# Kernel tuning notes

Hardware: AMD Instinct MI355X
Metric: run time of the kernel (lower is better)

## Reference

```python
import jax, jax.numpy as jnp
import numpy as np

B, N, DIM_IN, DIM_K, DIM_V, NH = 2, 2048, 1024, 1024, 1024, 16

def setup_inputs() -> dict:
    key = jax.random.key(0)
    ks = jax.random.split(key, 7)
    s_in = 1.0 / np.sqrt(DIM_IN)
    return {
        "x": jax.random.normal(ks[0], (B, N, DIM_IN), dtype=jnp.float32),
        "Wq": jax.random.uniform(ks[1], (DIM_IN, DIM_K), jnp.float32, -s_in, s_in),
        "bq": jax.random.uniform(ks[2], (DIM_K,), jnp.float32, -s_in, s_in),
        "Wk": jax.random.uniform(ks[3], (DIM_IN, DIM_K), jnp.float32, -s_in, s_in),
        "bk": jax.random.uniform(ks[4], (DIM_K,), jnp.float32, -s_in, s_in),
        "Wv": jax.random.uniform(ks[5], (DIM_IN, DIM_V), jnp.float32, -s_in, s_in),
        "bv": jax.random.uniform(ks[6], (DIM_V,), jnp.float32, -s_in, s_in),
    }

def reference(x, Wq, bq, Wk, bk, Wv, bv):
    b, n, _ = x.shape
    dk = DIM_K // NH
    dv = DIM_V // NH
    scale = 1.0 / np.sqrt(dk)
    # project and split heads: [b, nh, n, dk]
    q = (x @ Wq + bq).reshape(b, n, NH, dk).transpose(0, 2, 1, 3)
    k = (x @ Wk + bk).reshape(b, n, NH, dk).transpose(0, 2, 1, 3)
    v = (x @ Wv + bv).reshape(b, n, NH, dv).transpose(0, 2, 1, 3)
    dist = jnp.einsum('bhqd,bhkd->bhqk', q, k) * scale  # [b,nh,n,n]
    dist = jax.nn.softmax(dist, axis=-1)
    att = jnp.einsum('bhqk,bhkd->bhqd', dist, v)
    return att.transpose(0, 2, 1, 3).reshape(b, n, DIM_V)
```

## Files before the change

### kernel.cpp

```cpp
#include <hip/hip_runtime.h>

#define DI __device__ __forceinline__

typedef unsigned short u16;
typedef short short8 __attribute__((ext_vector_type(8)));
typedef float f32x4 __attribute__((ext_vector_type(4)));
typedef float f32x16 __attribute__((ext_vector_type(16)));
typedef u16 u16x4 __attribute__((ext_vector_type(4)));
typedef unsigned u32x4 __attribute__((ext_vector_type(4)));
typedef int i32x2 __attribute__((ext_vector_type(2)));

DI u16 f2bf(float f){
    unsigned u = __builtin_bit_cast(unsigned, f);
    u += 0x7FFFu + ((u >> 16) & 1u);
    return (u16)(u >> 16);
}

#if defined(__has_builtin)
#if __has_builtin(__builtin_amdgcn_global_load_lds)
#define HAS_GLL 1
#endif
#if __has_builtin(__builtin_amdgcn_exp2f)
#define HAS_EXP2 1
#endif
#if __has_builtin(__builtin_amdgcn_permlane32_swap)
#define HAS_PL32 1
#endif
#endif

DI void async16(u16* lds, const u16* g){
#ifdef HAS_GLL
    __builtin_amdgcn_global_load_lds(
        (const __attribute__((address_space(1))) unsigned int*)g,
        (__attribute__((address_space(3))) unsigned int*)lds, 16, 0, 0);
#else
    *(short8*)lds = *(const short8*)g;
#endif
}

DI float ex2(float x){
#ifdef HAS_EXP2
    return __builtin_amdgcn_exp2f(x);
#else
    return exp2f(x);
#endif
}

DI unsigned cvtpk(float lo, float hi){
    unsigned r;
    asm("v_cvt_pk_bf16_f32 %0, %1, %2" : "=v"(r) : "v"(lo), "v"(hi));
    return r;
}

DI i32x2 plswap(int a, int b){
#ifdef HAS_PL32
    return __builtin_amdgcn_permlane32_swap(a, b, false, false);
#else
    i32x2 r;
    int ax = __shfl_xor(a, 32), bx = __shfl_xor(b, 32);
    int hi = (threadIdx.x & 63) >> 5;
    r[0] = hi ? bx : a;
    r[1] = hi ? b : ax;
    return r;
#endif
}

#define SEQ   2048
#define DIN   1024
#define MTOT  4096
#define QSCALE 0.18033688011112042f
#define THR2   11.5f

__global__ void k_cvt_x(const float* __restrict__ x, u16* __restrict__ xb){
    int i = (blockIdx.x * 256 + threadIdx.x) * 4;
    f32x4 v = *(const f32x4*)(x + i);
    u16x4 o;
    for (int j = 0; j < 4; j++) o[j] = f2bf(v[j]);
    *(u16x4*)(xb + i) = o;
}

__global__ void k_tw3(const float* __restrict__ Wq, const float* __restrict__ Wk,
                      const float* __restrict__ Wv, u16* __restrict__ Wt3){
    const float* W = (blockIdx.z == 0) ? Wq : (blockIdx.z == 1) ? Wk : Wv;
    u16* Wt = Wt3 + (size_t)blockIdx.z * DIN * DIN;
    __shared__ float t[32][33];
    int tx = threadIdx.x, ty = threadIdx.y;
    int n0 = blockIdx.x * 32, k0 = blockIdx.y * 32;
    for (int i = 0; i < 4; i++)
        t[ty + i*8][tx] = W[(size_t)(k0 + ty + i*8) * DIN + n0 + tx];
    __syncthreads();
    for (int i = 0; i < 4; i++)
        Wt[(size_t)(n0 + ty + i*8) * DIN + k0 + tx] = f2bf(t[tx][ty + i*8]);
}

__global__ __launch_bounds__(256, 3) void k_projf(const u16* __restrict__ A,
                                                  const u16* __restrict__ Wt3,
                                                  const float* __restrict__ bq,
                                                  const float* __restrict__ bk,
                                                  const float* __restrict__ bv,
                                                  u16* __restrict__ qb,
                                                  u16* __restrict__ kb,
                                                  u16* __restrict__ vtb){
    __shared__ __align__(16) u16 As[3][4096];
    __shared__ __align__(16) u16 Bs[3][4096];
    int tid = threadIdx.x;
    int l = tid & 63, w = tid >> 6;
    int lq = l & 15, lg = l >> 4;
    int wm = w >> 1, wn = w & 1;
    int by  = blockIdx.y;
    int mat = by >> 3;
    int m0 = blockIdx.x * 128, n0 = (by & 7) * 128;
    const u16* Bt = Wt3 + (size_t)mat * DIN * DIN;
    const float* bias = (mat == 0) ? bq : (mat == 1) ? bk : bv;

    int r0 = tid >> 2, c0 = (tid & 3) * 8;
    const u16* ap0 = A  + (size_t)(m0 + r0)      * DIN + c0;
    const u16* ap1 = A  + (size_t)(m0 + 64 + r0) * DIN + c0;
    const u16* bp0 = Bt + (size_t)(n0 + r0)      * DIN + c0;
    const u16* bp1 = Bt + (size_t)(n0 + 64 + r0) * DIN + c0;
    int d0 = tid * 8, d1 = 2048 + tid * 8;

#define PSTAGE(bi) {                                              \
    async16(&As[bi][d0], ap0); async16(&As[bi][d1], ap1);         \
    async16(&Bs[bi][d0], bp0); async16(&Bs[bi][d1], bp1);         \
    ap0 += 32; ap1 += 32; bp0 += 32; bp1 += 32; }

    f32x4 acc[4][4] = {};
    PSTAGE(0)

    for (int t = 0; t < 32; t++){
        int cur = t % 3;
        if (t + 1 < 32){
            PSTAGE((t + 1) % 3)
            asm volatile("s_waitcnt vmcnt(4)" ::: "memory");
        } else {
            asm volatile("s_waitcnt vmcnt(0)" ::: "memory");
        }
        __builtin_amdgcn_s_barrier();

        short8 af[4], bf[4];
        #pragma unroll
        for (int f = 0; f < 4; f++){
            af[f] = *(const short8*)&As[cur][(wm*64 + f*16 + lq) * 32 + lg * 8];
            bf[f] = *(const short8*)&Bs[cur][(wn*64 + f*16 + lq) * 32 + lg * 8];
        }
        #pragma unroll
        for (int fm = 0; fm < 4; fm++)
            #pragma unroll
            for (int fn = 0; fn < 4; fn++)
                acc[fm][fn] = __builtin_amdgcn_mfma_f32_16x16x32_bf16(af[fm], bf[fn], acc[fm][fn], 0, 0, 0);
        __builtin_amdgcn_s_barrier();
    }
#undef PSTAGE

    for (int fn = 0; fn < 4; fn++){
        int cc = n0 + wn*64 + fn*16 + lq;
        float bvv = bias[cc];
        int h = cc >> 6, d = cc & 63;
        for (int fm = 0; fm < 4; fm++){
            int mbase = m0 + wm*64 + fm*16 + lg*4;
            int b = mbase >> 11, n = mbase & 2047;
            if (mat == 2){
                u16x4 pv;
                for (int r = 0; r < 4; r++) pv[r] = f2bf(acc[fm][fn][r] + bvv);
                *(u16x4*)&vtb[((size_t)(b*16 + h) * 64 + d) * SEQ + n] = pv;
            } else {
                u16* dst = (mat == 0) ? qb : kb;
                float sc = (mat == 0) ? QSCALE : 1.0f;
                for (int r = 0; r < 4; r++){
                    float v = (acc[fm][fn][r] + bvv) * sc;
                    dst[((size_t)(b*16 + h) * SEQ + (n + r)) * 64 + d] = f2bf(v);
                }
            }
        }
    }
}

#define MFMA32(a, b, c) __builtin_amdgcn_mfma_f32_32x32x16_bf16(a, b, c, 0, 0, 0)

#define MAKE_PA(dst, S, base) {                                   \
    unsigned a0 = cvtpk(S[base+0], S[base+1]);                    \
    unsigned a1 = cvtpk(S[base+2], S[base+3]);                    \
    unsigned b0 = cvtpk(S[base+4], S[base+5]);                    \
    unsigned b1 = cvtpk(S[base+6], S[base+7]);                    \
    i32x2 r0 = plswap((int)a0, (int)b0);                          \
    i32x2 r1 = plswap((int)a1, (int)b1);                          \
    u32x4 wv = {(unsigned)r0[0], (unsigned)r1[0],                 \
                (unsigned)r0[1], (unsigned)r1[1]};                \
    dst = __builtin_bit_cast(short8, wv); }

template<int SPLIT>
__global__ __launch_bounds__(256, 3) void k_attn(const u16* __restrict__ Q,
                                                 const u16* __restrict__ K,
                                                 const u16* __restrict__ Vt,
                                                 float* __restrict__ out,
                                                 float* __restrict__ po,
                                                 float* __restrict__ mls){
    __shared__ __align__(16) u16 Ks[3][64 * 64];
    __shared__ __align__(16) u16 Vs[3][64 * 64];

    int tid = threadIdx.x, l = tid & 63, w = tid >> 6;
    int lq = l & 31, hi = l >> 5;
    int bh = blockIdx.y;
    int b = bh >> 4, h = bh & 15;
    int q0 = blockIdx.x * 128 + w * 32;
    int sp = blockIdx.z;
    int kvb = sp * (SEQ / SPLIT);
    const int NT = (SEQ / SPLIT) / 64;

    const u16* Qb = Q  + (size_t)bh * SEQ * 64;
    const u16* Kb = K  + (size_t)bh * SEQ * 64;
    const u16* Vb = Vt + (size_t)bh * 64 * SEQ;

    int row0 = tid >> 3;
    int c0   = (tid & 7) ^ (row0 & 7);
    const u16* kp0 = Kb + (size_t)(kvb + row0)      * 64 + c0 * 8;
    const u16* kp1 = Kb + (size_t)(kvb + row0 + 32) * 64 + c0 * 8;
    const u16* vp0 = Vb + (size_t)row0        * SEQ + kvb + c0 * 8;
    const u16* vp1 = Vb + (size_t)(row0 + 32) * SEQ + kvb + c0 * 8;
    int d0 = tid * 8, d1 = 2048 + tid * 8;

#define STAGE(bi) {                                               \
    async16(&Ks[bi][d0], kp0); async16(&Ks[bi][d1], kp1);         \
    async16(&Vs[bi][d0], vp0); async16(&Vs[bi][d1], vp1);         \
    kp0 += 64*64; kp1 += 64*64; vp0 += 64; vp1 += 64; }

    short8 qf[4];
    #pragma unroll
    for (int ks = 0; ks < 4; ks++)
        qf[ks] = *(const short8*)(Qb + (size_t)(q0 + lq) * 64 + ks*16 + hi*8);

    STAGE(0)

    float m = -INFINITY, ls = 0.f;
    f32x16 o0 = {}, o1 = {};
    int rx = (lq & 7) << 4;

    for (int t = 0; t < NT; t++){
        int cur = t % 3;
        if (t + 1 < NT){
            STAGE((t + 1) % 3)
            asm volatile("s_waitcnt vmcnt(4)" ::: "memory");
        } else {
            asm volatile("s_waitcnt vmcnt(0)" ::: "memory");
        }
        __builtin_amdgcn_s_barrier();

        const char* kB = (const char*)&Ks[cur][0];
        const char* vB = (const char*)&Vs[cur][0];

        f32x16 st0 = {}, st1 = {};
        #pragma unroll
        for (int ks = 0; ks < 4; ks++){
            int cb = ((ks*2 + hi) << 4) ^ rx;
            short8 ka = *(const short8*)(kB + lq*128        + cb);
            short8 kb = *(const short8*)(kB + (32+lq)*128   + cb);
            st0 = MFMA32(ka, qf[ks], st0);
            st1 = MFMA32(kb, qf[ks], st1);
        }

        float p0 = fmaxf(st0[0], st1[0]), p1 = fmaxf(st0[1], st1[1]);
        float p2 = fmaxf(st0[2], st1[2]), p3 = fmaxf(st0[3], st1[3]);
        #pragma unroll
        for (int r = 4; r < 16; r += 4){
            p0 = fmaxf(p0, fmaxf(st0[r+0], st1[r+0]));
            p1 = fmaxf(p1, fmaxf(st0[r+1], st1[r+1]));
            p2 = fmaxf(p2, fmaxf(st0[r+2], st1[r+2]));
            p3 = fmaxf(p3, fmaxf(st0[r+3], st1[r+3]));
        }
        float pm = fmaxf(fmaxf(p0, p1), fmaxf(p2, p3));
        pm = fmaxf(pm, __shfl_xor(pm, 32));

        if (__any(pm > m + THR2)){
            float mn  = fmaxf(m, pm);
            float fac = ex2(m - mn);
            m = mn;
            ls *= fac;
            #pragma unroll
            for (int r = 0; r < 16; r++){
                int row = (r & 3) + 8*(r >> 2) + 4*hi;
                float f = __shfl(fac, row);
                o0[r] *= f; o1[r] *= f;
            }
        }

        float psum = 0.f;
        #pragma unroll
        for (int r = 0; r < 16; r++){
            st0[r] = ex2(st0[r] - m); psum += st0[r];
            st1[r] = ex2(st1[r] - m); psum += st1[r];
        }
        psum += __shfl_xor(psum, 32);
        ls += psum;

        short8 pa0, pa1, pa2, pa3;
        MAKE_PA(pa0, st0, 0)
        MAKE_PA(pa1, st0, 8)
        MAKE_PA(pa2, st1, 0)
        MAKE_PA(pa3, st1, 8)

        #pragma unroll
        for (int kct = 0; kct < 4; kct++){
            short8 pf = (kct == 0) ? pa0 : (kct == 1) ? pa1 : (kct == 2) ? pa2 : pa3;
            int cb = ((kct*2 + hi) << 4) ^ rx;
            short8 v0 = *(const short8*)(vB + lq*128      + cb);
            short8 v1 = *(const short8*)(vB + (32+lq)*128 + cb);
            o0 = MFMA32(pf, v0, o0);
            o1 = MFMA32(pf, v1, o1);
        }
        __builtin_amdgcn_s_barrier();
    }

    if (SPLIT == 1){
        #pragma unroll
        for (int r = 0; r < 16; r++){
            int row = (r & 3) + 8*(r >> 2) + 4*hi;
            float inv = 1.0f / __shfl(ls, row);
            float* op = out + ((size_t)b * SEQ + (q0 + row)) * 1024 + h*64 + lq;
            op[0]  = o0[r] * inv;
            op[32] = o1[r] * inv;
        }
    } else {
        float* pb = po + (size_t)sp * MTOT * 1024;
        #pragma unroll
        for (int r = 0; r < 16; r++){
            int row = (r & 3) + 8*(r >> 2) + 4*hi;
            float* op = pb + ((size_t)b * SEQ + (q0 + row)) * 1024 + h*64 + lq;
            op[0]  = o0[r];
            op[32] = o1[r];
        }
        if (hi == 0){
            float* mp = mls + (((size_t)sp*32 + bh) * SEQ + (q0 + lq)) * 2;
            mp[0] = m; mp[1] = ls;
        }
    }
#undef STAGE
}

template<int S>
__global__ __launch_bounds__(256) void k_comb(const float* __restrict__ po,
                                              const float* __restrict__ mls,
                                              float* __restrict__ out){
    size_t i = ((size_t)blockIdx.x * 256 + threadIdx.x) * 4;
    size_t row = i >> 10;
    int col = (int)(i & 1023);
    int b = (int)(row >> 11), n = (int)(row & 2047);
    int bh = b*16 + (col >> 6);

    float mv[S], lv[S], wv[S];
    float M = -INFINITY;
    #pragma unroll
    for (int s = 0; s < S; s++){
        const float* p = mls + (((size_t)s*32 + bh) * SEQ + n) * 2;
        mv[s] = p[0]; lv[s] = p[1];
        M = fmaxf(M, mv[s]);
    }
    float L = 0.f;
    #pragma unroll
    for (int s = 0; s < S; s++){ wv[s] = ex2(mv[s] - M); L += wv[s] * lv[s]; }
    float inv = 1.0f / L;
    f32x4 acc = {};
    #pragma unroll
    for (int s = 0; s < S; s++){
        f32x4 v = *(const f32x4*)(po + (size_t)s * MTOT * 1024 + i);
        acc += v * wv[s];
    }
    acc *= inv;
    *(f32x4*)(out + i) = acc;
}

extern "C" void kernel_launch(void* const* d_in, const int* in_sizes, int n_in,
                              void* d_out, int out_size, void* d_ws, size_t ws_size,
                              hipStream_t stream){
    const float* x  = (const float*)d_in[0];
    const float* Wq = (const float*)d_in[1];
    const float* bq = (const float*)d_in[2];
    const float* Wk = (const float*)d_in[3];
    const float* bk = (const float*)d_in[4];
    const float* Wv = (const float*)d_in[5];
    const float* bv = (const float*)d_in[6];
    float* out = (float*)d_out;

    const size_t MB = (size_t)1 << 20;
    if (ws_size < 38 * MB) return;

    char* ws = (char*)d_ws;
    u16* xb   = (u16*)(ws);
    u16* wt3  = (u16*)(ws +  8 * MB);
    u16* qb   = (u16*)(ws + 14 * MB);
    u16* kb   = (u16*)(ws + 22 * MB);
    u16* vtb  = (u16*)(ws + 30 * MB);
    int S = (ws_size >= 38 * MB + 2 * 17 * MB) ? 2 : 1;
    float* po  = (float*)(ws + 38 * MB);
    float* mls = (float*)(ws + 38 * MB + (size_t)S * 16 * MB);

    k_cvt_x<<<4096, 256, 0, stream>>>(x, xb);
    k_tw3<<<dim3(32, 32, 3), dim3(32, 8), 0, stream>>>(Wq, Wk, Wv, wt3);

    k_projf<<<dim3(32, 24), 256, 0, stream>>>(xb, wt3, bq, bk, bv, qb, kb, vtb);

    if (S == 2){
        k_attn<2><<<dim3(16, 32, 2), 256, 0, stream>>>(qb, kb, vtb, out, po, mls);
        k_comb<2><<<4096, 256, 0, stream>>>(po, mls, out);
    } else {
        k_attn<1><<<dim3(16, 32, 1), 256, 0, stream>>>(qb, kb, vtb, out, po, mls);
    }
}
```

Measured before the change: 111.8 us.

## Double-buffer attention KV tiles, raise occupancy, add MFMA priority hints

Shrinks the attention kernel's shared K/V ring from three buffers to two, which lowers LDS use and allows the launch bound to target four blocks per SM instead of three. The loop now uses one barrier per iteration, with a full vmcnt wait at the end of each iteration. It also wraps the MFMA sections of both the projection GEMM and attention in s_setprio hints, and pairs up the softmax partial sums into a two-wide vector. The trade-off is less prefetch depth, since each tile's load must complete before the end-of-iteration barrier.

New measurement: 109.9 us. About the same (-1.7%).

```diff
diff --git a/kernel.cpp b/kernel.cpp
--- a/kernel.cpp
+++ b/kernel.cpp
@@ -4,6 +4,7 @@
 
 typedef unsigned short u16;
 typedef short short8 __attribute__((ext_vector_type(8)));
+typedef float f32x2 __attribute__((ext_vector_type(2)));
 typedef float f32x4 __attribute__((ext_vector_type(4)));
 typedef float f32x16 __attribute__((ext_vector_type(16)));
 typedef u16 u16x4 __attribute__((ext_vector_type(4)));
@@ -144,11 +145,13 @@
             af[f] = *(const short8*)&As[cur][(wm*64 + f*16 + lq) * 32 + lg * 8];
             bf[f] = *(const short8*)&Bs[cur][(wn*64 + f*16 + lq) * 32 + lg * 8];
         }
+        __builtin_amdgcn_s_setprio(1);
         #pragma unroll
         for (int fm = 0; fm < 4; fm++)
             #pragma unroll
             for (int fn = 0; fn < 4; fn++)
                 acc[fm][fn] = __builtin_amdgcn_mfma_f32_16x16x32_bf16(af[fm], bf[fn], acc[fm][fn], 0, 0, 0);
+        __builtin_amdgcn_s_setprio(0);
         __builtin_amdgcn_s_barrier();
     }
 #undef PSTAGE
@@ -190,14 +193,14 @@
     dst = __builtin_bit_cast(short8, wv); }
 
 template<int SPLIT>
-__global__ __launch_bounds__(256, 3) void k_attn(const u16* __restrict__ Q,
+__global__ __launch_bounds__(256, 4) void k_attn(const u16* __restrict__ Q,
                                                  const u16* __restrict__ K,
                                                  const u16* __restrict__ Vt,
                                                  float* __restrict__ out,
                                                  float* __restrict__ po,
                                                  float* __restrict__ mls){
-    __shared__ __align__(16) u16 Ks[3][64 * 64];
-    __shared__ __align__(16) u16 Vs[3][64 * 64];
+    __shared__ __align__(16) u16 Ks[2][64 * 64];
+    __shared__ __align__(16) u16 Vs[2][64 * 64];
 
     int tid = threadIdx.x, l = tid & 63, w = tid >> 6;
     int lq = l & 31, hi = l >> 5;
@@ -237,19 +240,19 @@
     int rx = (lq & 7) << 4;
 
     for (int t = 0; t < NT; t++){
-        int cur = t % 3;
-        if (t + 1 < NT){
-            STAGE((t + 1) % 3)
-            asm volatile("s_waitcnt vmcnt(4)" ::: "memory");
-        } else {
-            asm volatile("s_waitcnt vmcnt(0)" ::: "memory");
-        }
-        __builtin_amdgcn_s_barrier();
+        int cur = t & 1;
+        if (t + 1 < NT) STAGE(cur ^ 1)
+        if (t == 0){
+            if (NT > 1) asm volatile("s_waitcnt vmcnt(4)" ::: "memory");
+            else        asm volatile("s_waitcnt vmcnt(0)" ::: "memory");
+            __builtin_amdgcn_s_barrier();
+        }
 
         const char* kB = (const char*)&Ks[cur][0];
         const char* vB = (const char*)&Vs[cur][0];
 
         f32x16 st0 = {}, st1 = {};
+        __builtin_amdgcn_s_setprio(1);
         #pragma unroll
         for (int ks = 0; ks < 4; ks++){
             int cb = ((ks*2 + hi) << 4) ^ rx;
@@ -258,6 +261,7 @@
             st0 = MFMA32(ka, qf[ks], st0);
             st1 = MFMA32(kb, qf[ks], st1);
         }
+        __builtin_amdgcn_s_setprio(0);
 
         float p0 = fmaxf(st0[0], st1[0]), p1 = fmaxf(st0[1], st1[1]);
         float p2 = fmaxf(st0[2], st1[2]), p3 = fmaxf(st0[3], st1[3]);
@@ -284,12 +288,18 @@
             }
         }
 
-        float psum = 0.f;
-        #pragma unroll
-        for (int r = 0; r < 16; r++){
-            st0[r] = ex2(st0[r] - m); psum += st0[r];
-            st1[r] = ex2(st1[r] - m); psum += st1[r];
-        }
+        f32x2 ps = {0.f, 0.f};
+        #pragma unroll
+        for (int r = 0; r < 16; r += 2){
+            st0[r]   = ex2(st0[r]   - m);
+            st0[r+1] = ex2(st0[r+1] - m);
+            st1[r]   = ex2(st1[r]   - m);
+            st1[r+1] = ex2(st1[r+1] - m);
+            f32x2 a = {st0[r], st0[r+1]};
+            f32x2 c = {st1[r], st1[r+1]};
+            ps += a + c;
+        }
+        float psum = ps[0] + ps[1];
         psum += __shfl_xor(psum, 32);
         ls += psum;
 
@@ -299,6 +309,7 @@
         MAKE_PA(pa2, st1, 0)
         MAKE_PA(pa3, st1, 8)
 
+        __builtin_amdgcn_s_setprio(1);
         #pragma unroll
         for (int kct = 0; kct < 4; kct++){
             short8 pf = (kct == 0) ? pa0 : (kct == 1) ? pa1 : (kct == 2) ? pa2 : pa3;
@@ -308,6 +319,9 @@
             o0 = MFMA32(pf, v0, o0);
             o1 = MFMA32(pf, v1, o1);
         }
+        __builtin_amdgcn_s_setprio(0);
+
+        asm volatile("s_waitcnt vmcnt(0)" ::: "memory");
         __builtin_amdgcn_s_barrier();
     }
 
```
